# Kernel tuning notes

Hardware: AMD Instinct MI355X
Metric: run time of the kernel (lower is better)

Reference implementation:

```python
import jax, jax.numpy as jnp
import numpy as np

N, M, C_IN, C_OUT = 16384, 8192, 128, 64
P_EDGE = 0.005  # ~41 hyperedges per vertex


def setup_inputs() -> dict:
    key = jax.random.key(0)
    k1, k2, k3, k4 = jax.random.split(key, 4)
    X = jax.random.normal(k1, (N, C_IN), dtype=jnp.float32)
    # 0/1 incidence matrix (dense realization of a sparse hypergraph)
    H = (jax.random.uniform(k2, (N, M)) < P_EDGE).astype(jnp.float32)
    W = jax.random.normal(k3, (C_OUT, C_IN), dtype=jnp.float32) / np.sqrt(C_IN)
    b = jax.random.normal(k4, (C_OUT,), dtype=jnp.float32) * 0.01
    return {"X": X, "H": H, "W": W, "b": b}


def reference(X, H, W, b):
    # theta: linear projection  (N, C_in) -> (N, C_out)
    Xt = X @ W.T + b
    # D_v^{-1/2} and D_e^{-1} with torch-style nan_to_num semantics
    dv = jnp.nan_to_num(jnp.power(H.sum(axis=1), -0.5))  # (N,)
    de = jnp.nan_to_num(jnp.power(H.sum(axis=0), -1.0))  # (M,)
    # L @ X = diag(dv) H diag(de) H^T diag(dv) @ Xt, applied as row scalings
    # (W_e is the identity in the original code)
    Y = dv[:, None] * Xt           # (N, C_out)
    Y = H.T @ Y                    # (M, C_out) gather to hyperedges
    Y = de[:, None] * Y            # (M, C_out)
    Y = H @ Y                      # (N, C_out) scatter back to vertices
    Y = dv[:, None] * Y            # (N, C_out)
    # is_last=False -> ReLU; bn=None; dropout is identity in eval mode
    return jax.nn.relu(Y)
```

## Files before the change

kernel.cpp:

```cpp
#include <hip/hip_runtime.h>
#include <hip/hip_bf16.h>
#include <stdint.h>

#define N_V   16384
#define M_E   8192
#define CIN   128
#define COUT  64
#define RCAP  128
#define CCAP  192
#define BCAP  16

#define OFF_ROWCNT  0
#define OFF_COLCNT  (N_V * 4)
#define OFF_ROWLIST (OFF_COLCNT + M_E * 4)
#define OFF_COLLIST (OFF_ROWLIST + N_V * RCAP * 2)
#define OFF_YV      (OFF_COLLIST + M_E * CCAP * 2)
#define OFF_E       (OFF_YV + N_V * COUT * 4)

__global__ __launch_bounds__(256) void k_rows(
    const uint4* __restrict__ H4,
    int* __restrict__ row_cnt, unsigned short* __restrict__ row_list,
    int* __restrict__ col_cnt, unsigned short* __restrict__ col_list) {
  __shared__ unsigned short bucket[4][BCAP + 1][64];
  int wid  = threadIdx.x >> 6;
  int lane = threadIdx.x & 63;
  int n    = blockIdx.x * 4 + wid;
  const uint4* rp = H4 + (size_t)n * (M_E / 4) + lane;
  unsigned short (*bk)[64] = bucket[wid];
  int cnt = 0;
  int mb  = lane * 4;
#pragma unroll 8
  for (int it = 0; it < (M_E / 4) / 64; ++it) {
    uint4 v = rp[it * 64];
    int w;
    w = cnt > BCAP ? BCAP : cnt; bk[w][lane] = (unsigned short)(mb + 0); cnt += (v.x != 0u);
    w = cnt > BCAP ? BCAP : cnt; bk[w][lane] = (unsigned short)(mb + 1); cnt += (v.y != 0u);
    w = cnt > BCAP ? BCAP : cnt; bk[w][lane] = (unsigned short)(mb + 2); cnt += (v.z != 0u);
    w = cnt > BCAP ? BCAP : cnt; bk[w][lane] = (unsigned short)(mb + 3); cnt += (v.w != 0u);
    mb += 256;
  }
  if (cnt > BCAP) cnt = BCAP;
  int pfx = cnt;
#pragma unroll
  for (int s = 1; s < 64; s <<= 1) {
    int t = __shfl_up(pfx, s, 64);
    if (lane >= s) pfx += t;
  }
  int total = __shfl(pfx, 63, 64);
  int start = pfx - cnt;
  unsigned short* rl = row_list + n * RCAP;
  for (int k = 0; k < cnt; ++k) {
    int p = start + k;
    int e = bk[k][lane];
    if (p < RCAP) rl[p] = (unsigned short)e;
    int cp = atomicAdd(&col_cnt[e], 1);
    if (cp < CCAP) col_list[e * CCAP + cp] = (unsigned short)n;
  }
  if (lane == 63) row_cnt[n] = total > RCAP ? RCAP : total;
}

__global__ __launch_bounds__(256) void k_project(
    const float* __restrict__ X, const float* __restrict__ W,
    const float* __restrict__ b, const int* __restrict__ row_cnt,
    float* __restrict__ Yv) {
  int wid  = threadIdx.x >> 6;
  int lane = threadIdx.x & 63;
  int cb   = __builtin_amdgcn_readfirstlane(wid);
  int n    = blockIdx.x * 64 + lane;
  const float* xrow  = X + n * CIN;
  const float* wbase = W + cb * 16 * CIN;

  float acc[16];
#pragma unroll
  for (int j = 0; j < 16; ++j) acc[j] = 0.f;

  for (int k4 = 0; k4 < CIN / 4; ++k4) {
    float4 x = *(const float4*)(xrow + k4 * 4);
#pragma unroll
    for (int j = 0; j < 16; ++j) {
      float4 w = *(const float4*)(wbase + j * CIN + k4 * 4);
      acc[j] += x.x * w.x + x.y * w.y + x.z * w.z + x.w * w.w;
    }
  }

  int cnt  = row_cnt[n];
  float dv = cnt > 0 ? rsqrtf((float)cnt) : 0.f;
  float* yrow = Yv + n * COUT + cb * 16;
#pragma unroll
  for (int g = 0; g < 4; ++g) {
    float4 o;
    o.x = dv * (acc[4 * g + 0] + b[cb * 16 + 4 * g + 0]);
    o.y = dv * (acc[4 * g + 1] + b[cb * 16 + 4 * g + 1]);
    o.z = dv * (acc[4 * g + 2] + b[cb * 16 + 4 * g + 2]);
    o.w = dv * (acc[4 * g + 3] + b[cb * 16 + 4 * g + 3]);
    *(float4*)(yrow + 4 * g) = o;
  }
}

__global__ __launch_bounds__(256) void k_edge(
    const float* __restrict__ Yv, const int* __restrict__ col_cnt,
    const unsigned short* __restrict__ col_list, float* __restrict__ E) {
  int wid  = threadIdx.x >> 6;
  int lane = threadIdx.x & 63;
  int m    = blockIdx.x * 4 + wid;
  int realcnt = col_cnt[m];
  int cnt  = realcnt > CCAP ? CCAP : realcnt;
  const unsigned short* lst = col_list + m * CCAP;
  float acc = 0.f;
  int i = 0;
  for (; i + 8 <= cnt; i += 8) {
    uint4 u = *(const uint4*)(lst + i);
    int n0 = u.x & 0xffff, n1 = u.x >> 16;
    int n2 = u.y & 0xffff, n3 = u.y >> 16;
    int n4 = u.z & 0xffff, n5 = u.z >> 16;
    int n6 = u.w & 0xffff, n7 = u.w >> 16;
    float a0 = Yv[n0 * COUT + lane];
    float a1 = Yv[n1 * COUT + lane];
    float a2 = Yv[n2 * COUT + lane];
    float a3 = Yv[n3 * COUT + lane];
    float a4 = Yv[n4 * COUT + lane];
    float a5 = Yv[n5 * COUT + lane];
    float a6 = Yv[n6 * COUT + lane];
    float a7 = Yv[n7 * COUT + lane];
    acc += ((a0 + a1) + (a2 + a3)) + ((a4 + a5) + (a6 + a7));
  }
  for (; i < cnt; ++i) acc += Yv[(int)lst[i] * COUT + lane];
  float den = realcnt > 0 ? 1.f / (float)realcnt : 0.f;
  E[m * COUT + lane] = den * acc;
}

__global__ __launch_bounds__(256) void k_vertex(
    const float* __restrict__ E, const int* __restrict__ row_cnt,
    const unsigned short* __restrict__ row_list, float* __restrict__ out) {
  int wid  = threadIdx.x >> 6;
  int lane = threadIdx.x & 63;
  int n    = blockIdx.x * 4 + wid;
  int cnt  = row_cnt[n];
  const unsigned short* lst = row_list + n * RCAP;
  float acc = 0.f;
  int i = 0;
  for (; i + 8 <= cnt; i += 8) {
    uint4 u = *(const uint4*)(lst + i);
    int m0 = u.x & 0xffff, m1 = u.x >> 16;
    int m2 = u.y & 0xffff, m3 = u.y >> 16;
    int m4 = u.z & 0xffff, m5 = u.z >> 16;
    int m6 = u.w & 0xffff, m7 = u.w >> 16;
    float a0 = E[m0 * COUT + lane];
    float a1 = E[m1 * COUT + lane];
    float a2 = E[m2 * COUT + lane];
    float a3 = E[m3 * COUT + lane];
    float a4 = E[m4 * COUT + lane];
    float a5 = E[m5 * COUT + lane];
    float a6 = E[m6 * COUT + lane];
    float a7 = E[m7 * COUT + lane];
    acc += ((a0 + a1) + (a2 + a3)) + ((a4 + a5) + (a6 + a7));
  }
  for (; i < cnt; ++i) acc += E[(int)lst[i] * COUT + lane];
  float dv = cnt > 0 ? rsqrtf((float)cnt) : 0.f;
  out[n * COUT + lane] = fmaxf(dv * acc, 0.f);
}

extern "C" void kernel_launch(void* const* d_in, const int* in_sizes, int n_in,
                              void* d_out, int out_size, void* d_ws, size_t ws_size,
                              hipStream_t stream) {
  const float* X = (const float*)d_in[0];
  const float* H = (const float*)d_in[1];
  const float* W = (const float*)d_in[2];
  const float* b = (const float*)d_in[3];
  float* out = (float*)d_out;

  char* ws = (char*)d_ws;
  int* row_cnt = (int*)(ws + OFF_ROWCNT);
  int* col_cnt = (int*)(ws + OFF_COLCNT);
  unsigned short* row_list = (unsigned short*)(ws + OFF_ROWLIST);
  unsigned short* col_list = (unsigned short*)(ws + OFF_COLLIST);
  float* Yv = (float*)(ws + OFF_YV);
  float* E  = (float*)(ws + OFF_E);

  hipMemsetAsync(col_cnt, 0, M_E * 4, stream);

  k_rows<<<N_V / 4, 256, 0, stream>>>((const uint4*)H, row_cnt, row_list,
                                      col_cnt, col_list);
  k_project<<<N_V / 64, 256, 0, stream>>>(X, W, b, row_cnt, Yv);
  k_edge<<<M_E / 4, 256, 0, stream>>>(Yv, col_cnt, col_list, E);
  k_vertex<<<N_V / 4, 256, 0, stream>>>(E, row_cnt, row_list, out);
}
```

Measured before the change: 737.7 us.

## Build column lists via staged band histogram, prefix and scatter instead of global atomics

Global atomicAdd on col_cnt per nonzero is replaced by a three-pass counting sort. Nonzeros are first staged per workgroup in LDS, then per-band LDS histograms are built, a column-wise prefix over bands is taken, and the edge lists are scattered using LDS atomics. This removes contended global atomics and the memset, and makes the column list order deterministic. In exchange it adds three kernel launches and extra workspace traffic for the partial and offset tables (about 8 MB).

```diff
diff --git a/kernel.cpp b/kernel.cpp
--- a/kernel.cpp
+++ b/kernel.cpp
@@ -1,5 +1,4 @@
 #include <hip/hip_runtime.h>
-#include <hip/hip_bf16.h>
 #include <stdint.h>
 
 #define N_V   16384
@@ -9,21 +8,33 @@
 #define RCAP  128
 #define CCAP  192
 #define BCAP  16
+#define SCAP4 256
+#define NWG1  (N_V / 4)
+#define NBAND 256
+#define WPB   16
 
 #define OFF_ROWCNT  0
-#define OFF_COLCNT  (N_V * 4)
+#define OFF_COLCNT  (OFF_ROWCNT + N_V * 4)
 #define OFF_ROWLIST (OFF_COLCNT + M_E * 4)
 #define OFF_COLLIST (OFF_ROWLIST + N_V * RCAP * 2)
-#define OFF_YV      (OFF_COLLIST + M_E * CCAP * 2)
+#define OFF_PART    (OFF_COLLIST + M_E * CCAP * 2)
+#define OFF_OFFT    (OFF_PART + NBAND * M_E * 2)
+#define OFF_STAGED  (OFF_OFFT + NBAND * M_E * 2)
+#define OFF_STGCNT  (OFF_STAGED + NWG1 * SCAP4 * 4)
+#define OFF_YV      (OFF_STGCNT + NWG1 * 4)
 #define OFF_E       (OFF_YV + N_V * COUT * 4)
 
 __global__ __launch_bounds__(256) void k_rows(
     const uint4* __restrict__ H4,
     int* __restrict__ row_cnt, unsigned short* __restrict__ row_list,
-    int* __restrict__ col_cnt, unsigned short* __restrict__ col_list) {
+    unsigned int* __restrict__ staged, int* __restrict__ staged_cnt) {
   __shared__ unsigned short bucket[4][BCAP + 1][64];
-  int wid  = threadIdx.x >> 6;
-  int lane = threadIdx.x & 63;
+  __shared__ unsigned int ls_stage[SCAP4];
+  __shared__ int ls_n;
+  int wid  = threadIdx.x >> 6;
+  int lane = threadIdx.x & 63;
+  if (threadIdx.x == 0) ls_n = 0;
+  __syncthreads();
   int n    = blockIdx.x * 4 + wid;
   const uint4* rp = H4 + (size_t)n * (M_E / 4) + lane;
   unsigned short (*bk)[64] = bucket[wid];
@@ -53,10 +64,68 @@
     int p = start + k;
     int e = bk[k][lane];
     if (p < RCAP) rl[p] = (unsigned short)e;
-    int cp = atomicAdd(&col_cnt[e], 1);
-    if (cp < CCAP) col_list[e * CCAP + cp] = (unsigned short)n;
+    int sp = atomicAdd(&ls_n, 1);
+    if (sp < SCAP4) ls_stage[sp] = ((unsigned int)e << 6) | (unsigned int)(n & 63);
   }
   if (lane == 63) row_cnt[n] = total > RCAP ? RCAP : total;
+  __syncthreads();
+  int sn = ls_n; if (sn > SCAP4) sn = SCAP4;
+  for (int j = threadIdx.x; j < sn; j += 256)
+    staged[blockIdx.x * SCAP4 + j] = ls_stage[j];
+  if (threadIdx.x == 0) staged_cnt[blockIdx.x] = sn;
+}
+
+__global__ __launch_bounds__(256) void k_hist(
+    const unsigned int* __restrict__ staged, const int* __restrict__ staged_cnt,
+    unsigned short* __restrict__ partial) {
+  __shared__ unsigned int hist[M_E];
+  for (int j = threadIdx.x; j < M_E; j += 256) hist[j] = 0;
+  __syncthreads();
+  int b = blockIdx.x;
+  for (int w = 0; w < WPB; ++w) {
+    int wg = b * WPB + w;
+    int c  = staged_cnt[wg];
+    for (int j = threadIdx.x; j < c; j += 256)
+      atomicAdd(&hist[staged[wg * SCAP4 + j] >> 6], 1u);
+  }
+  __syncthreads();
+  for (int j = threadIdx.x; j < M_E; j += 256)
+    partial[b * M_E + j] = (unsigned short)hist[j];
+}
+
+__global__ __launch_bounds__(64) void k_prefix(
+    const unsigned short* __restrict__ partial,
+    unsigned short* __restrict__ offt, int* __restrict__ col_cnt) {
+  int e = blockIdx.x * 64 + threadIdx.x;
+  int run = 0;
+#pragma unroll 8
+  for (int b = 0; b < NBAND; ++b) {
+    int v = partial[b * M_E + e];
+    offt[b * M_E + e] = (unsigned short)run;
+    run += v;
+  }
+  col_cnt[e] = run;
+}
+
+__global__ __launch_bounds__(256) void k_scatter(
+    const unsigned int* __restrict__ staged, const int* __restrict__ staged_cnt,
+    const unsigned short* __restrict__ offt,
+    unsigned short* __restrict__ col_list) {
+  __shared__ unsigned int off_l[M_E];
+  int b = blockIdx.x;
+  for (int j = threadIdx.x; j < M_E; j += 256) off_l[j] = offt[b * M_E + j];
+  __syncthreads();
+  for (int w = 0; w < WPB; ++w) {
+    int wg = b * WPB + w;
+    int c  = staged_cnt[wg];
+    for (int j = threadIdx.x; j < c; j += 256) {
+      unsigned int s = staged[wg * SCAP4 + j];
+      int e  = (int)(s >> 6);
+      int nl = (int)(s & 63u);
+      int slot = (int)atomicAdd(&off_l[e], 1u);
+      if (slot < CCAP) col_list[e * CCAP + slot] = (unsigned short)(b * 64 + nl);
+    }
+  }
 }
 
 __global__ __launch_bounds__(256) void k_project(
@@ -174,13 +243,18 @@
   int* col_cnt = (int*)(ws + OFF_COLCNT);
   unsigned short* row_list = (unsigned short*)(ws + OFF_ROWLIST);
   unsigned short* col_list = (unsigned short*)(ws + OFF_COLLIST);
+  unsigned short* partial  = (unsigned short*)(ws + OFF_PART);
+  unsigned short* offt     = (unsigned short*)(ws + OFF_OFFT);
+  unsigned int*   staged   = (unsigned int*)(ws + OFF_STAGED);
+  int*            stg_cnt  = (int*)(ws + OFF_STGCNT);
   float* Yv = (float*)(ws + OFF_YV);
   float* E  = (float*)(ws + OFF_E);
 
-  hipMemsetAsync(col_cnt, 0, M_E * 4, stream);
-
-  k_rows<<<N_V / 4, 256, 0, stream>>>((const uint4*)H, row_cnt, row_list,
-                                      col_cnt, col_list);
+  k_rows<<<NWG1, 256, 0, stream>>>((const uint4*)H, row_cnt, row_list,
+                                   staged, stg_cnt);
+  k_hist<<<NBAND, 256, 0, stream>>>(staged, stg_cnt, partial);
+  k_prefix<<<M_E / 64, 64, 0, stream>>>(partial, offt, col_cnt);
+  k_scatter<<<NBAND, 256, 0, stream>>>(staged, stg_cnt, offt, col_list);
   k_project<<<N_V / 64, 256, 0, stream>>>(X, W, b, row_cnt, Yv);
   k_edge<<<M_E / 4, 256, 0, stream>>>(Yv, col_cnt, col_list, E);
   k_vertex<<<N_V / 4, 256, 0, stream>>>(E, row_cnt, row_list, out);
```

New measurement: 755.9 us. 1.02x slower.
